# Kernel optimization log

Hardware: AMD Instinct MI355X
Metric: run time of the kernel (lower is better)

## Reference

```python
import jax, jax.numpy as jnp
import numpy as np

B, T, C, H = 2, 2048, 1024, 16
HD = C // H  # 64


def _rope(x, cos, sin):
    # x: [B, T, H, HD]; cos/sin: [T, HD//2]
    xr = x.reshape(*x.shape[:-1], HD // 2, 2)
    xre, xim = xr[..., 0], xr[..., 1]
    c = cos[None, :, None, :]
    s = sin[None, :, None, :]
    out_re = xre * c - xim * s
    out_im = xre * s + xim * c
    return jnp.stack([out_re, out_im], axis=-1).reshape(x.shape)


def setup_inputs() -> dict:
    key = jax.random.key(0)
    ks = jax.random.split(key, 4)
    x = jax.random.normal(ks[0], (B, T, C), dtype=jnp.float32)
    W_qkv = jax.random.normal(ks[1], (3 * C, C), dtype=jnp.float32) * (C ** -0.5)
    W_proj = jax.random.normal(ks[2], (C, C), dtype=jnp.float32) * (C ** -0.5)
    b_proj = jnp.zeros((C,), dtype=jnp.float32)
    # standard RoPE frequencies, theta=10000
    inv_freq = 1.0 / (10000.0 ** (np.arange(0, HD, 2, dtype=np.float32) / HD))
    angles = np.outer(np.arange(T, dtype=np.float32), inv_freq)  # [T, HD/2]
    freqs_cos = jnp.asarray(np.cos(angles), dtype=jnp.float32)
    freqs_sin = jnp.asarray(np.sin(angles), dtype=jnp.float32)
    return {"x": x, "freqs_cos": freqs_cos, "freqs_sin": freqs_sin,
            "W_qkv": W_qkv, "W_proj": W_proj, "b_proj": b_proj}


def reference(x, freqs_cos, freqs_sin, W_qkv, W_proj, b_proj):
    qkv = x @ W_qkv.T                       # [B, T, 3C]
    q, k, v = jnp.split(qkv, 3, axis=-1)
    q = q.reshape(B, T, H, HD)
    k = k.reshape(B, T, H, HD)
    v = v.reshape(B, T, H, HD)
    q = _rope(q, freqs_cos, freqs_sin)
    k = _rope(k, freqs_cos, freqs_sin)
    # [B, H, T, HD]
    q = q.transpose(0, 2, 1, 3)
    k = k.transpose(0, 2, 1, 3)
    v = v.transpose(0, 2, 1, 3)
    att = jnp.einsum('bhqd,bhkd->bhqk', q, k) * (HD ** -0.5)
    causal = jnp.tril(jnp.ones((T, T), dtype=bool))
    att = jnp.where(causal[None, None], att, -jnp.inf)
    att = jax.nn.softmax(att, axis=-1)
    out = jnp.einsum('bhqk,bhkd->bhqd', att, v)
    out = out.transpose(0, 2, 1, 3).reshape(B, T, C)
    return out @ W_proj.T + b_proj
```

## Files before the change

kernel.cpp:

```cpp
#include <hip/hip_runtime.h>


typedef short  bf16x8 __attribute__((ext_vector_type(8)));
typedef float  f32x4  __attribute__((ext_vector_type(4)));
typedef unsigned short u16x4 __attribute__((ext_vector_type(4)));

#define B_  2
#define T_  2048
#define H_  16
#define HD_ 64
#define NINF (-__builtin_inff())

static __device__ __forceinline__ unsigned short f2bf(float f) {
    union { float f; unsigned u; } v; v.f = f;
    unsigned r = v.u + 0x7fffu + ((v.u >> 16) & 1u);
    return (unsigned short)(r >> 16);
}

#define GLOAD_LDS16(gp, lp)                                                              \
    __builtin_amdgcn_global_load_lds((const __attribute__((address_space(1))) void*)(gp), \
                                     (__attribute__((address_space(3))) void*)(lp), 16, 0, 0)

__global__ void convert3(const float* __restrict__ x, const float* __restrict__ wqkv,
                         const float* __restrict__ wproj,
                         unsigned short* __restrict__ xb, unsigned short* __restrict__ wqkvb,
                         unsigned short* __restrict__ wprojb) {
    int i = blockIdx.x * blockDim.x + threadIdx.x;
    const float* src; unsigned short* dst; int off;
    if (i < 1048576)      { src = x;     dst = xb;     off = i; }
    else if (i < 1835008) { src = wqkv;  dst = wqkvb;  off = i - 1048576; }
    else                  { src = wproj; dst = wprojb; off = i - 1835008; }
    float4 f = ((const float4*)src)[off];
    u16x4 o; o[0] = f2bf(f.x); o[1] = f2bf(f.y); o[2] = f2bf(f.z); o[3] = f2bf(f.w);
    ((u16x4*)dst)[off] = o;
}

__global__ __launch_bounds__(256) void gemm_qkv(const unsigned short* __restrict__ A,
                                                const unsigned short* __restrict__ Bm,
                                                const float* __restrict__ fa,
                                                const float* __restrict__ fb,
                                                unsigned short* __restrict__ Qo,
                                                unsigned short* __restrict__ Ko,
                                                unsigned short* __restrict__ Vt) {
    __shared__ __align__(16) unsigned short As[2][4096];
    __shared__ __align__(16) unsigned short Bs[2][4096];
    const int K = 1024;
    const int tid  = threadIdx.x;
    const int w    = tid >> 6;
    const int lane = tid & 63;
    const int r    = lane & 15, g = lane >> 4;
    const int m0   = blockIdx.y * 128;
    const int n0   = blockIdx.x * 128;
    const int wm   = (w >> 1) * 64, wn = (w & 1) * 64;

    f32x4 acc[4][4];
#pragma unroll
    for (int i = 0; i < 4; i++)
#pragma unroll
        for (int j = 0; j < 4; j++) acc[i][j] = (f32x4){0.f, 0.f, 0.f, 0.f};

    const int u0 = tid, u1 = 256 + tid;
    const unsigned short* ga0 = A  + (size_t)(m0 + (u0 >> 2)) * K + (u0 & 3) * 8;
    const unsigned short* ga1 = A  + (size_t)(m0 + (u1 >> 2)) * K + (u1 & 3) * 8;
    const unsigned short* gb0 = Bm + (size_t)(n0 + (u0 >> 2)) * K + (u0 & 3) * 8;
    const unsigned short* gb1 = Bm + (size_t)(n0 + (u1 >> 2)) * K + (u1 & 3) * 8;
    const int lws = w * 512;

#define STAGE_G(bb, k0_)                                            \
    do {                                                            \
        GLOAD_LDS16(ga0 + (k0_), &As[bb][lws]);                     \
        GLOAD_LDS16(ga1 + (k0_), &As[bb][2048 + lws]);              \
        GLOAD_LDS16(gb0 + (k0_), &Bs[bb][lws]);                     \
        GLOAD_LDS16(gb1 + (k0_), &Bs[bb][2048 + lws]);              \
    } while (0)

    STAGE_G(0, 0);
    __syncthreads();

    for (int k0 = 0; k0 < K; k0 += 32) {
        const int cur = (k0 >> 5) & 1;
        if (k0 + 32 < K) STAGE_G(cur ^ 1, k0 + 32);

        bf16x8 a[4], b[4];
#pragma unroll
        for (int mi = 0; mi < 4; mi++) a[mi] = *(const bf16x8*)&As[cur][(wm + mi * 16 + r) * 32 + 8 * g];
#pragma unroll
        for (int ni = 0; ni < 4; ni++) b[ni] = *(const bf16x8*)&Bs[cur][(wn + ni * 16 + r) * 32 + 8 * g];
#pragma unroll
        for (int mi = 0; mi < 4; mi++)
#pragma unroll
            for (int ni = 0; ni < 4; ni++)
                acc[mi][ni] = __builtin_amdgcn_mfma_f32_16x16x32_bf16(a[mi], b[ni], acc[mi][ni], 0, 0, 0);

        __syncthreads();
    }
#undef STAGE_G

    const float* fcos = (fa[0] > 0.5f) ? fa : fb;
    const float* fsin = (fa[0] > 0.5f) ? fb : fa;
    const int region = n0 >> 10;

    if (region < 2) {
        unsigned short* dst = region ? Ko : Qo;
        const float sgn = (r & 1) ? 1.f : -1.f;
#pragma unroll
        for (int mi = 0; mi < 4; mi++) {
            int row0 = m0 + wm + mi * 16 + 4 * g;
            int b    = row0 >> 11;
            int t0   = row0 & 2047;
#pragma unroll
            for (int ni = 0; ni < 4; ni++) {
                int nn = (n0 & 1023) + wn + ni * 16 + r;
                int h  = nn >> 6, dd = nn & 63;
                int i  = dd >> 1;
                size_t obase = ((size_t)((b * 16 + h) * 2048 + t0)) * 64 + dd;
#pragma unroll
                for (int j = 0; j < 4; j++) {
                    float c = fcos[(t0 + j) * 32 + i];
                    float s = fsin[(t0 + j) * 32 + i];
                    float v  = acc[mi][ni][j];
                    float vp = __shfl_xor(v, 1);
                    float out = __builtin_fmaf(sgn * vp, s, v * c);
                    dst[obase + (size_t)j * 64] = f2bf(out);
                }
            }
        }
    } else {
#pragma unroll
        for (int mi = 0; mi < 4; mi++) {
            int row0 = m0 + wm + mi * 16 + 4 * g;
            int b    = row0 >> 11;
            int t0   = row0 & 2047;
            int tp   = (t0 & ~31) + 8 * ((t0 & 15) >> 2) + 4 * ((t0 & 31) >> 4);
#pragma unroll
            for (int ni = 0; ni < 4; ni++) {
                int nn = (n0 & 1023) + wn + ni * 16 + r;
                int h  = nn >> 6, dd = nn & 63;
                u16x4 ov;
#pragma unroll
                for (int j = 0; j < 4; j++) ov[j] = f2bf(acc[mi][ni][j]);
                *(u16x4*)(Vt + ((size_t)((b * 16 + h) * 64 + dd)) * 2048 + tp) = ov;
            }
        }
    }
}

__global__ __launch_bounds__(256) void gemm_nt(const unsigned short* __restrict__ A,
                                               const unsigned short* __restrict__ Bm,
                                               float* __restrict__ Cm,
                                               const float* __restrict__ bias,
                                               int M, int N, int K) {
    __shared__ __align__(16) unsigned short As[2][4096];
    __shared__ __align__(16) unsigned short Bs[2][4096];
    const int tid  = threadIdx.x;
    const int w    = tid >> 6;
    const int lane = tid & 63;
    const int r    = lane & 15, g = lane >> 4;
    const int m0   = blockIdx.y * 128;
    const int n0   = blockIdx.x * 128;
    const int wm   = (w >> 1) * 64, wn = (w & 1) * 64;

    f32x4 acc[4][4];
#pragma unroll
    for (int i = 0; i < 4; i++)
#pragma unroll
        for (int j = 0; j < 4; j++) acc[i][j] = (f32x4){0.f, 0.f, 0.f, 0.f};

    const int u0 = tid, u1 = 256 + tid;
    const unsigned short* ga0 = A  + (size_t)(m0 + (u0 >> 2)) * K + (u0 & 3) * 8;
    const unsigned short* ga1 = A  + (size_t)(m0 + (u1 >> 2)) * K + (u1 & 3) * 8;
    const unsigned short* gb0 = Bm + (size_t)(n0 + (u0 >> 2)) * K + (u0 & 3) * 8;
    const unsigned short* gb1 = Bm + (size_t)(n0 + (u1 >> 2)) * K + (u1 & 3) * 8;
    const int lws = w * 512;

#define STAGE_G(bb, k0_)                                            \
    do {                                                            \
        GLOAD_LDS16(ga0 + (k0_), &As[bb][lws]);                     \
        GLOAD_LDS16(ga1 + (k0_), &As[bb][2048 + lws]);              \
        GLOAD_LDS16(gb0 + (k0_), &Bs[bb][lws]);                     \
        GLOAD_LDS16(gb1 + (k0_), &Bs[bb][2048 + lws]);              \
    } while (0)

    STAGE_G(0, 0);
    __syncthreads();

    for (int k0 = 0; k0 < K; k0 += 32) {
        const int cur = (k0 >> 5) & 1;
        if (k0 + 32 < K) STAGE_G(cur ^ 1, k0 + 32);

        bf16x8 a[4], b[4];
#pragma unroll
        for (int mi = 0; mi < 4; mi++) a[mi] = *(const bf16x8*)&As[cur][(wm + mi * 16 + r) * 32 + 8 * g];
#pragma unroll
        for (int ni = 0; ni < 4; ni++) b[ni] = *(const bf16x8*)&Bs[cur][(wn + ni * 16 + r) * 32 + 8 * g];
#pragma unroll
        for (int mi = 0; mi < 4; mi++)
#pragma unroll
            for (int ni = 0; ni < 4; ni++)
                acc[mi][ni] = __builtin_amdgcn_mfma_f32_16x16x32_bf16(a[mi], b[ni], acc[mi][ni], 0, 0, 0);

        __syncthreads();
    }
#undef STAGE_G

#pragma unroll
    for (int mi = 0; mi < 4; mi++) {
        int row = m0 + wm + mi * 16 + 4 * g;
#pragma unroll
        for (int ni = 0; ni < 4; ni++) {
            int col = n0 + wn + ni * 16 + r;
            float bv = bias[col];
#pragma unroll
            for (int j = 0; j < 4; j++)
                Cm[(size_t)(row + j) * N + col] = acc[mi][ni][j] + bv;
        }
    }
}

static __device__ __forceinline__ int swzb(int row, int chunk) {
    return (row << 7) + ((chunk ^ (row & 7)) << 4);
}

template <bool DIAG>
static __device__ __forceinline__ void softmax64(const f32x4 s[4], int key0, int qrow,
                                                 float& m, float& l,
                                                 f32x4 o[4], bf16x8& pf0, bf16x8& pf1, int g) {
    const float SCL = 0.125f * 1.4426950408889634f;
    float sv[16];
#pragma unroll
    for (int ks = 0; ks < 4; ks++)
#pragma unroll
        for (int j = 0; j < 4; j++) {
            float x = s[ks][j];
            if (DIAG && (key0 + ks * 16 + 4 * g + j > qrow)) x = NINF;
            sv[ks * 4 + j] = x;
        }
    float t8[8];
#pragma unroll
    for (int i = 0; i < 8; i++) t8[i] = fmaxf(sv[i], sv[i + 8]);
#pragma unroll
    for (int i = 0; i < 4; i++) t8[i] = fmaxf(t8[i], t8[i + 4]);
    float tm = fmaxf(fmaxf(t8[0], t8[1]), fmaxf(t8[2], t8[3]));
    tm = fmaxf(tm, __shfl_xor(tm, 16));
    tm = fmaxf(tm, __shfl_xor(tm, 32));

    float msc;
    if (__all(tm <= m)) {
        msc = m * SCL;
    } else {
        float mnew  = fmaxf(m, tm);
        float alpha = __builtin_amdgcn_exp2f((m - mnew) * SCL);
        l *= alpha;
#pragma unroll
        for (int ch = 0; ch < 4; ch++) o[ch] *= alpha;
        m = mnew;
        msc = mnew * SCL;
    }
    float p[16];
#pragma unroll
    for (int i = 0; i < 16; i++) p[i] = __builtin_amdgcn_exp2f(__builtin_fmaf(sv[i], SCL, -msc));
    float ps0 = ((p[0] + p[1]) + (p[2] + p[3])) + ((p[4] + p[5]) + (p[6] + p[7]));
    float ps1 = ((p[8] + p[9]) + (p[10] + p[11])) + ((p[12] + p[13]) + (p[14] + p[15]));
    l += ps0 + ps1;
    union { unsigned w[4]; bf16x8 v; } q0, q1;
    asm("v_cvt_pk_bf16_f32 %0, %1, %2" : "=v"(q0.w[0]) : "v"(p[0]),  "v"(p[1]));
    asm("v_cvt_pk_bf16_f32 %0, %1, %2" : "=v"(q0.w[1]) : "v"(p[2]),  "v"(p[3]));
    asm("v_cvt_pk_bf16_f32 %0, %1, %2" : "=v"(q0.w[2]) : "v"(p[4]),  "v"(p[5]));
    asm("v_cvt_pk_bf16_f32 %0, %1, %2" : "=v"(q0.w[3]) : "v"(p[6]),  "v"(p[7]));
    asm("v_cvt_pk_bf16_f32 %0, %1, %2" : "=v"(q1.w[0]) : "v"(p[8]),  "v"(p[9]));
    asm("v_cvt_pk_bf16_f32 %0, %1, %2" : "=v"(q1.w[1]) : "v"(p[10]), "v"(p[11]));
    asm("v_cvt_pk_bf16_f32 %0, %1, %2" : "=v"(q1.w[2]) : "v"(p[12]), "v"(p[13]));
    asm("v_cvt_pk_bf16_f32 %0, %1, %2" : "=v"(q1.w[3]) : "v"(p[14]), "v"(p[15]));
    pf0 = q0.v; pf1 = q1.v;
}

__global__ __launch_bounds__(256, 4) void attn_fwd(const unsigned short* __restrict__ Q,
                                                   const unsigned short* __restrict__ Kk,
                                                   const unsigned short* __restrict__ Vt,
                                                   unsigned short* __restrict__ O) {
    __shared__ __align__(16) unsigned short Ks[2][4096];
    __shared__ __align__(16) unsigned short Vs[2][4096];

    const int w    = threadIdx.x >> 6;
    const int lane = threadIdx.x & 63;
    const int l15  = lane & 15, g = lane >> 4;

    const int bid = blockIdx.x;
    const int x   = bid & 7;
    const int y   = (bid >> 3) & 31;
    const int q   = bid >> 8;
    const int bh  = x | ((y & 3) << 3);
    const int z   = y >> 2;
    const int r   = (q == 0) ? z : (q == 1) ? 15 - z : (q == 2) ? 16 + z : 31 - z;
    const int b   = bh >> 4, h = bh & 15;

    const unsigned short* Qb = Q  + (size_t)bh * T_ * HD_;
    const unsigned short* Kb = Kk + (size_t)bh * T_ * HD_;
    const unsigned short* Vb = Vt + (size_t)bh * HD_ * T_;

    const int qrow = r * 64 + 16 * w + l15;
    bf16x8 qf0 = *(const bf16x8*)(Qb + (size_t)qrow * 64 + 8 * g);
    bf16x8 qf1 = *(const bf16x8*)(Qb + (size_t)qrow * 64 + 32 + 8 * g);

    f32x4 o[4];
#pragma unroll
    for (int ch = 0; ch < 4; ch++) o[ch] = (f32x4){0, 0, 0, 0};
    float m2 = NINF, lsum = 0.f;

    int off[4][2];
#pragma unroll
    for (int i = 0; i < 4; i++) {
        off[i][0] = swzb(16 * i + l15, g);
        off[i][1] = swzb(16 * i + l15, 4 + g);
    }

    const int t   = threadIdx.x;
    const int r0  = t >> 3;
    const int cs  = (t & 7) ^ (r0 & 7);
    const int t8e = t * 8;
    const unsigned short* sK = Kb + (size_t)r0 * 64 + cs * 8;
    const unsigned short* sV = Vb + (size_t)r0 * 2048 + cs * 8;

#define STAGE_TILE(bb, key0_)                                                   \
    do {                                                                        \
        GLOAD_LDS16(sK + (size_t)(key0_) * 64,        &Ks[bb][t8e]);            \
        GLOAD_LDS16(sK + (size_t)((key0_) + 32) * 64, &Ks[bb][2048 + t8e]);     \
        GLOAD_LDS16(sV + (key0_),                     &Vs[bb][t8e]);            \
        GLOAD_LDS16(sV + 32 * 2048 + (key0_),         &Vs[bb][2048 + t8e]);     \
    } while (0)

    STAGE_TILE(0, 0);
    __syncthreads();

#pragma unroll 2
    for (int kt = 0; kt <= r; ++kt) {
        const int key0 = kt * 64;
        const int cur  = kt & 1;
        if (kt < r) STAGE_TILE(cur ^ 1, key0 + 64);

        const char* KsB = (const char*)&Ks[cur][0];
        const char* VsB = (const char*)&Vs[cur][0];

        bf16x8 kf[4][2], va[4][2];
#pragma unroll
        for (int i = 0; i < 4; i++) {
            kf[i][0] = *(const bf16x8*)(KsB + off[i][0]);
            kf[i][1] = *(const bf16x8*)(KsB + off[i][1]);
            va[i][0] = *(const bf16x8*)(VsB + off[i][0]);
            va[i][1] = *(const bf16x8*)(VsB + off[i][1]);
        }

        f32x4 z4 = (f32x4){0, 0, 0, 0};
        f32x4 s[4];
#pragma unroll
        for (int ks = 0; ks < 4; ks++) {
            s[ks] = __builtin_amdgcn_mfma_f32_16x16x32_bf16(kf[ks][0], qf0, z4, 0, 0, 0);
            s[ks] = __builtin_amdgcn_mfma_f32_16x16x32_bf16(kf[ks][1], qf1, s[ks], 0, 0, 0);
        }

        bf16x8 pf0, pf1;
        if (kt == r) softmax64<true >(s, key0, qrow, m2, lsum, o, pf0, pf1, g);
        else         softmax64<false>(s, key0, qrow, m2, lsum, o, pf0, pf1, g);

#pragma unroll
        for (int ch = 0; ch < 4; ch++) {
            o[ch] = __builtin_amdgcn_mfma_f32_16x16x32_bf16(va[ch][0], pf0, o[ch], 0, 0, 0);
            o[ch] = __builtin_amdgcn_mfma_f32_16x16x32_bf16(va[ch][1], pf1, o[ch], 0, 0, 0);
        }

        __syncthreads();
    }
#undef STAGE_TILE

    lsum += __shfl_xor(lsum, 16);
    lsum += __shfl_xor(lsum, 32);
    float inv = 1.f / lsum;

    size_t obase = (((size_t)b * T_ + qrow) * H_ + h) * HD_;
#pragma unroll
    for (int ch = 0; ch < 4; ch++) {
        int d0 = 16 * ch + 4 * g;
        u16x4 ov;
#pragma unroll
        for (int jj = 0; jj < 4; jj++) ov[jj] = f2bf(o[ch][jj] * inv);
        *(u16x4*)(O + obase + d0) = ov;
    }
}

extern "C" void kernel_launch(void* const* d_in, const int* in_sizes, int n_in,
                              void* d_out, int out_size, void* d_ws, size_t ws_size,
                              hipStream_t stream) {
    (void)out_size;
    const float *x = nullptr, *wqkv = nullptr, *wproj = nullptr, *bproj = nullptr;
    const float *fa = nullptr, *fb = nullptr;
    for (int i = 0; i < n_in; i++) {
        switch (in_sizes[i]) {
            case 4194304: x     = (const float*)d_in[i]; break;
            case 3145728: wqkv  = (const float*)d_in[i]; break;
            case 1048576: wproj = (const float*)d_in[i]; break;
            case 1024:    bproj = (const float*)d_in[i]; break;
            case 65536:   if (!fa) fa = (const float*)d_in[i]; else fb = (const float*)d_in[i]; break;
            default: break;
        }
    }
    if (!x || !wqkv || !wproj || !bproj || !fa || !fb) return;
    if (ws_size < (size_t)48 * 1024 * 1024) return;

    char* ws = (char*)d_ws;
    const size_t MB = 1024 * 1024;
    unsigned short* xb     = (unsigned short*)(ws);
    unsigned short* wqkvb  = (unsigned short*)(ws + 8  * MB);
    unsigned short* wprojb = (unsigned short*)(ws + 14 * MB);
    unsigned short* qro    = (unsigned short*)(ws + 16 * MB);
    unsigned short* kro    = (unsigned short*)(ws + 24 * MB);
    unsigned short* vt     = (unsigned short*)(ws + 32 * MB);
    unsigned short* oat    = (unsigned short*)(ws + 40 * MB);

    convert3<<<8192, 256, 0, stream>>>(x, wqkv, wproj, xb, wqkvb, wprojb);

    gemm_qkv<<<dim3(24, 32), 256, 0, stream>>>(xb, wqkvb, fa, fb, qro, kro, vt);

    attn_fwd<<<1024, 256, 0, stream>>>(qro, kro, vt, oat);

    gemm_nt<<<dim3(8, 32), 256, 0, stream>>>(oat, wprojb, (float*)d_out, bproj,
                                             4096, 1024, 1024);
}
```

Measured before the change: 131.8 us.

## Triple-buffer GEMM LDS staging with one barrier per k-step

Both projection GEMMs now keep three LDS buffers instead of two and prefetch two k-tiles ahead. Each iteration waits only on the older outstanding loads (vmcnt(4)) and issues a single barrier, replacing the prior two-sync pattern. The aim is to hide global-to-LDS latency and cut barrier stalls. It raises LDS use to 48KB per block, which may reduce occupancy.

```diff
diff --git a/kernel.cpp b/kernel.cpp
--- a/kernel.cpp
+++ b/kernel.cpp
@@ -35,6 +35,7 @@
     ((u16x4*)dst)[off] = o;
 }
 
+
 __global__ __launch_bounds__(256) void gemm_qkv(const unsigned short* __restrict__ A,
                                                 const unsigned short* __restrict__ Bm,
                                                 const float* __restrict__ fa,
@@ -42,9 +43,9 @@
                                                 unsigned short* __restrict__ Qo,
                                                 unsigned short* __restrict__ Ko,
                                                 unsigned short* __restrict__ Vt) {
-    __shared__ __align__(16) unsigned short As[2][4096];
-    __shared__ __align__(16) unsigned short Bs[2][4096];
-    const int K = 1024;
+    __shared__ __align__(16) unsigned short As[3][4096];
+    __shared__ __align__(16) unsigned short Bs[3][4096];
+    const int K = 1024, NT = 32;
     const int tid  = threadIdx.x;
     const int w    = tid >> 6;
     const int lane = tid & 63;
@@ -74,27 +75,35 @@
         GLOAD_LDS16(gb1 + (k0_), &Bs[bb][2048 + lws]);              \
     } while (0)
 
+#define COMPUTE_T(bb)                                                                        \
+    do {                                                                                     \
+        bf16x8 a[4], b[4];                                                                   \
+        _Pragma("unroll")                                                                    \
+        for (int mi = 0; mi < 4; mi++) a[mi] = *(const bf16x8*)&As[bb][(wm + mi * 16 + r) * 32 + 8 * g]; \
+        _Pragma("unroll")                                                                    \
+        for (int ni = 0; ni < 4; ni++) b[ni] = *(const bf16x8*)&Bs[bb][(wn + ni * 16 + r) * 32 + 8 * g]; \
+        _Pragma("unroll")                                                                    \
+        for (int mi = 0; mi < 4; mi++)                                                       \
+            _Pragma("unroll")                                                                \
+            for (int ni = 0; ni < 4; ni++)                                                   \
+                acc[mi][ni] = __builtin_amdgcn_mfma_f32_16x16x32_bf16(a[mi], b[ni], acc[mi][ni], 0, 0, 0); \
+    } while (0)
+
     STAGE_G(0, 0);
-    __syncthreads();
-
-    for (int k0 = 0; k0 < K; k0 += 32) {
-        const int cur = (k0 >> 5) & 1;
-        if (k0 + 32 < K) STAGE_G(cur ^ 1, k0 + 32);
-
-        bf16x8 a[4], b[4];
-#pragma unroll
-        for (int mi = 0; mi < 4; mi++) a[mi] = *(const bf16x8*)&As[cur][(wm + mi * 16 + r) * 32 + 8 * g];
-#pragma unroll
-        for (int ni = 0; ni < 4; ni++) b[ni] = *(const bf16x8*)&Bs[cur][(wn + ni * 16 + r) * 32 + 8 * g];
-#pragma unroll
-        for (int mi = 0; mi < 4; mi++)
-#pragma unroll
-            for (int ni = 0; ni < 4; ni++)
-                acc[mi][ni] = __builtin_amdgcn_mfma_f32_16x16x32_bf16(a[mi], b[ni], acc[mi][ni], 0, 0, 0);
-
-        __syncthreads();
-    }
+    STAGE_G(1, 32);
+    for (int it = 0; it < NT - 1; ++it) {
+        asm volatile("s_waitcnt vmcnt(4)" ::: "memory");
+        __builtin_amdgcn_s_barrier();
+        __builtin_amdgcn_sched_barrier(0);
+        if (it + 2 < NT) STAGE_G((it + 2) % 3, (it + 2) * 32);
+        COMPUTE_T(it % 3);
+    }
+    asm volatile("s_waitcnt vmcnt(0)" ::: "memory");
+    __builtin_amdgcn_s_barrier();
+    __builtin_amdgcn_sched_barrier(0);
+    COMPUTE_T((NT - 1) % 3);
 #undef STAGE_G
+#undef COMPUTE_T
 
     const float* fcos = (fa[0] > 0.5f) ? fa : fb;
     const float* fsin = (fa[0] > 0.5f) ? fb : fa;
@@ -150,8 +159,8 @@
                                                float* __restrict__ Cm,
                                                const float* __restrict__ bias,
                                                int M, int N, int K) {
-    __shared__ __align__(16) unsigned short As[2][4096];
-    __shared__ __align__(16) unsigned short Bs[2][4096];
+    __shared__ __align__(16) unsigned short As[3][4096];
+    __shared__ __align__(16) unsigned short Bs[3][4096];
     const int tid  = threadIdx.x;
     const int w    = tid >> 6;
     const int lane = tid & 63;
@@ -159,6 +168,7 @@
     const int m0   = blockIdx.y * 128;
     const int n0   = blockIdx.x * 128;
     const int wm   = (w >> 1) * 64, wn = (w & 1) * 64;
+    const int NT   = K >> 5;
 
     f32x4 acc[4][4];
 #pragma unroll
@@ -181,27 +191,35 @@
         GLOAD_LDS16(gb1 + (k0_), &Bs[bb][2048 + lws]);              \
     } while (0)
 
+#define COMPUTE_T(bb)                                                                        \
+    do {                                                                                     \
+        bf16x8 a[4], b[4];                                                                   \
+        _Pragma("unroll")                                                                    \
+        for (int mi = 0; mi < 4; mi++) a[mi] = *(const bf16x8*)&As[bb][(wm + mi * 16 + r) * 32 + 8 * g]; \
+        _Pragma("unroll")                                                                    \
+        for (int ni = 0; ni < 4; ni++) b[ni] = *(const bf16x8*)&Bs[bb][(wn + ni * 16 + r) * 32 + 8 * g]; \
+        _Pragma("unroll")                                                                    \
+        for (int mi = 0; mi < 4; mi++)                                                       \
+            _Pragma("unroll")                                                                \
+            for (int ni = 0; ni < 4; ni++)                                                   \
+                acc[mi][ni] = __builtin_amdgcn_mfma_f32_16x16x32_bf16(a[mi], b[ni], acc[mi][ni], 0, 0, 0); \
+    } while (0)
+
     STAGE_G(0, 0);
-    __syncthreads();
-
-    for (int k0 = 0; k0 < K; k0 += 32) {
-        const int cur = (k0 >> 5) & 1;
-        if (k0 + 32 < K) STAGE_G(cur ^ 1, k0 + 32);
-
-        bf16x8 a[4], b[4];
-#pragma unroll
-        for (int mi = 0; mi < 4; mi++) a[mi] = *(const bf16x8*)&As[cur][(wm + mi * 16 + r) * 32 + 8 * g];
-#pragma unroll
-        for (int ni = 0; ni < 4; ni++) b[ni] = *(const bf16x8*)&Bs[cur][(wn + ni * 16 + r) * 32 + 8 * g];
-#pragma unroll
-        for (int mi = 0; mi < 4; mi++)
-#pragma unroll
-            for (int ni = 0; ni < 4; ni++)
-                acc[mi][ni] = __builtin_amdgcn_mfma_f32_16x16x32_bf16(a[mi], b[ni], acc[mi][ni], 0, 0, 0);
-
-        __syncthreads();
-    }
+    STAGE_G(1, 32);
+    for (int it = 0; it < NT - 1; ++it) {
+        asm volatile("s_waitcnt vmcnt(4)" ::: "memory");
+        __builtin_amdgcn_s_barrier();
+        __builtin_amdgcn_sched_barrier(0);
+        if (it + 2 < NT) STAGE_G((it + 2) % 3, (it + 2) * 32);
+        COMPUTE_T(it % 3);
+    }
+    asm volatile("s_waitcnt vmcnt(0)" ::: "memory");
+    __builtin_amdgcn_s_barrier();
+    __builtin_amdgcn_sched_barrier(0);
+    COMPUTE_T((NT - 1) % 3);
 #undef STAGE_G
+#undef COMPUTE_T
 
 #pragma unroll
     for (int mi = 0; mi < 4; mi++) {
```

Result: no change. 133.4 us (+1.2%).
